# Performance work log

Hardware: AMD Instinct MI355X
Metric: run time of the kernel (lower is better)

Reference implementation:

```python
import jax, jax.numpy as jnp
import numpy as np

B, CIN, OUT = 16, 64, 64
CH = CIN // 2          # depthwise group count (32)
H, W = 256, 256        # mas resolution; cen is at (H//2, W//2)

# The 8 fixed 3x3 dilation-3 kernels are center-minus-shifted-neighbor ops.
# Cross-correlation offsets (dy, dx) of the -1 tap, dilation 3:
OFFSETS = [(-3, -3), (-3, 0), (-3, 3), (0, 3), (3, 3), (3, 0), (3, -3), (0, -3)]


def setup_inputs() -> dict:
    key = jax.random.key(0)
    ks = jax.random.split(key, 9)
    cen = jax.random.normal(ks[0], (B, CIN, H // 2, W // 2), jnp.float32)
    mas = jax.random.normal(ks[1], (B, CH, H, W), jnp.float32)
    # inp_layer: Conv2d(CH, CH, k=3, s=2, p=1) + SiLU
    w_inp = jax.random.normal(ks[2], (CH, CH, 3, 3), jnp.float32) * 0.05
    b_inp = jax.random.normal(ks[3], (CH,), jnp.float32) * 0.05
    # layer1/2/3: grouped 1x1, groups=CH, per-group 8 in -> 2 out; store as [CH, 2, 8]
    w1 = jax.random.normal(ks[4], (CH, 2, 8), jnp.float32) * 0.1
    w2 = jax.random.normal(ks[5], (CH, 2, 8), jnp.float32) * 0.1
    w3 = jax.random.normal(ks[6], (CH, 2, 8), jnp.float32) * 0.1
    # out_conv: 1x1 conv, 3*CIN -> OUT, with bias
    w_out = jax.random.normal(ks[7], (OUT, 3 * CIN), jnp.float32) * 0.05
    b_out = jax.random.normal(ks[8], (OUT,), jnp.float32) * 0.05
    return {"cen": cen, "mas": mas, "w_inp": w_inp, "b_inp": b_inp,
            "w1": w1, "w2": w2, "w3": w3, "w_out": w_out, "b_out": b_out}


def _forward(cen, mas, w_inp, b_inp, w1, w2, w3, w_out, b_out):
    # stem: 3x3 stride-2 conv + SiLU  -> [B, CH, H//2, W//2]
    x = jax.lax.conv_general_dilated(
        mas, w_inp, window_strides=(2, 2), padding=((1, 1), (1, 1)),
        dimension_numbers=("NCHW", "OIHW", "NCHW"))
    x = jax.nn.silu(x + b_inp[None, :, None, None])
    b, c, h, w = x.shape
    # 8 dilated depthwise diff-convs == center minus zero-padded shifted copy
    xp = jnp.pad(x, ((0, 0), (0, 0), (3, 3), (3, 3)))
    deltas = jnp.stack(
        [x - jax.lax.dynamic_slice(xp, (0, 0, 3 + dy, 3 + dx), (b, c, h, w))
         for dy, dx in OFFSETS], axis=2)                     # [B, CH, 8, h, w]
    # grouped 1x1 gating convs (groups=CH): per-group [2,8] matmul
    g1 = jnp.einsum("bcdhw,cod->bcohw", deltas, w1)
    g2 = jnp.einsum("bcdhw,cod->bcohw", deltas, w2)
    square = (g1 * g2).reshape(b, 2 * c, h, w)               # layer1 * layer2
    dout = jnp.einsum("bcdhw,cod->bcohw", deltas, w3).reshape(b, 2 * c, h, w)
    # concat [square, dout, cen] along channels -> 1x1 out_conv
    outs = jnp.concatenate([square, dout, cen], axis=1)      # [B, 3*CIN, h, w]
    return jnp.einsum("bchw,oc->bohw", outs, w_out) + b_out[None, :, None, None]


def reference(cen, mas, w_inp, b_inp, w1, w2, w3, w_out, b_out):
    return _forward(cen, mas, w_inp, b_inp, w1, w2, w3, w_out, b_out)
```

## Files before the change

kernel.cpp:

```cpp
#include <hip/hip_runtime.h>
#include <hip/hip_bf16.h>

#define BATCH 16
#define CH    32
#define CIN   64
#define OUTC  64
#define HH    128
#define WW    128
#define HW    (HH * WW)
#define MHW   65536

typedef __attribute__((ext_vector_type(8))) short bf16x8;
typedef __attribute__((ext_vector_type(4))) float f32x4;

__device__ inline unsigned short bf16u(float x) {
  union { __hip_bfloat16 h; unsigned short s; } u;
  u.h = __float2bfloat16(x);
  return u.s;
}
__device__ inline unsigned int pack2(float lo, float hi) {
  return (unsigned int)bf16u(lo) | ((unsigned int)bf16u(hi) << 16);
}
__device__ inline float losf(unsigned u) { return __uint_as_float(u << 16); }
__device__ inline float hisf(unsigned u) { return __uint_as_float(u & 0xffff0000u); }

__global__ __launch_bounds__(256) void k_prep_weights(
    const float* __restrict__ w_out, const float* __restrict__ w_inp,
    const float* __restrict__ w3,
    unsigned short* __restrict__ wfrag, unsigned short* __restrict__ wfrag2,
    unsigned short* __restrict__ wfrag3) {
  int t = blockIdx.x * 256 + threadIdx.x;
  if (t < 9 * 2 * 64 * 8) {
    int e    = t & 7;
    int lane = (t >> 3) & 63;
    int ct   = (t >> 9) & 1;
    int tap  = t >> 10;
    int co = ct * 16 + (lane & 15);
    int ci = (lane >> 4) * 8 + e;
    wfrag[t] = bf16u(w_inp[(co * CH + ci) * 9 + tap]);
  }
  int t2 = t - 9216;
  if (t2 >= 0 && t2 < 8192) {
    int e    = t2 & 7;
    int lane = (t2 >> 3) & 63;
    int ot   = (t2 >> 9) & 3;
    int kt   = t2 >> 11;
    int o = ot * 16 + (lane & 15);
    int k = kt * 32 + (lane >> 4) * 8 + e;
    int col = (k < 64) ? k : 64 + k;
    wfrag2[t2] = bf16u(w_out[o * 192 + col]);
  }
  int t3 = t - 17408;
  if (t3 >= 0 && t3 < 18432) {
    int e    = t3 & 7;
    int lane = (t3 >> 3) & 63;
    int ot   = (t3 >> 9) & 3;
    int tap  = t3 >> 11;
    int o = ot * 16 + (lane & 15);
    int C = (lane >> 4) * 8 + e;
    const int kmap[9] = {0, 1, 2, 7, -1, 3, 6, 5, 4};
    float v = 0.f;
    if (tap == 4) {
      for (int k = 0; k < 8; ++k)
        for (int op = 0; op < 2; ++op)
          v += w_out[o * 192 + 64 + 2 * C + op] * w3[C * 16 + op * 8 + k];
    } else {
      int k = kmap[tap];
      for (int op = 0; op < 2; ++op)
        v -= w_out[o * 192 + 64 + 2 * C + op] * w3[C * 16 + op * 8 + k];
    }
    wfrag3[t3] = bf16u(v);
  }
}

__global__ __launch_bounds__(256) void k_prep_mas(
    const float* __restrict__ mas, unsigned short* __restrict__ masb) {
  __shared__ alignas(16) unsigned short tile[256 * 36];

  const int W = blockIdx.x + 256 * blockIdx.y;
  const int F = (W & 7) * 512 + (W >> 3);
  const int r = F & 255;
  const int b = F >> 8;
  const int t = threadIdx.x;

  const float* gp = mas + (size_t)b * CH * MHW + (size_t)r * 256 + t;
#pragma unroll 8
  for (int q = 0; q < 16; ++q) {
    float v0 = gp[(size_t)(2 * q) * MHW];
    float v1 = gp[(size_t)(2 * q + 1) * MHW];
    *(unsigned*)&tile[t * 36 + 2 * q] = pack2(v0, v1);
  }
  __syncthreads();

  unsigned short* op = masb + (((size_t)b * 256 + r) * 256) * 32;
#pragma unroll
  for (int it = 0; it < 4; ++it) {
    int idx = it * 256 + t;
    int px = idx >> 2, seg = idx & 3;
    uint2 a  = *(const uint2*)&tile[px * 36 + seg * 8];
    uint2 bq = *(const uint2*)&tile[px * 36 + seg * 8 + 4];
    *(uint4*)(op + (size_t)px * 32 + seg * 8) = make_uint4(a.x, a.y, bq.x, bq.y);
  }
}

#define SPITCH 36

__global__ __launch_bounds__(256, 3) void k_stem(
    const unsigned short* __restrict__ masb,
    const unsigned short* __restrict__ wfrag,
    const float* __restrict__ b_inp, unsigned short* __restrict__ xbuf) {
  __shared__ alignas(16) unsigned short xs[585 * SPITCH];

  const int W = blockIdx.x + 4 * blockIdx.y + 128 * blockIdx.z;
  const int F = (W & 7) * 256 + (W >> 3);
  const int bx = F & 3;
  const int by = (F >> 2) & 31;
  const int b  = F >> 7;

  const int t  = threadIdx.x;
  const int lane = t & 63;
  const int w = t >> 6;
  const int ct = w >> 1, chh = w & 1;

  const int I0 = by * 4, J0 = bx * 32;
  const int R0 = 2 * I0 - 1, C0 = 2 * J0 - 1;

  bf16x8 af[9];
#pragma unroll
  for (int tap = 0; tap < 9; ++tap)
    af[tap] = ((const bf16x8*)wfrag)[(tap * 2 + ct) * 64 + lane];

  const unsigned short* mb = masb + (size_t)b * 256 * 256 * 32;
  for (int idx = t; idx < 585 * 4; idx += 256) {
    int px = idx >> 2, seg = idx & 3;
    int rr = px / 65, cc = px - rr * 65;
    int gr = R0 + rr, gc = C0 + cc;
    uint4 v = make_uint4(0u, 0u, 0u, 0u);
    if (gr >= 0 && gc >= 0)
      v = *(const uint4*)(mb + ((size_t)gr * 256 + gc) * 32 + seg * 8);
    unsigned short* sp = xs + px * SPITCH + seg * 8;
    *(uint2*)(sp)     = make_uint2(v.x, v.y);
    *(uint2*)(sp + 4) = make_uint2(v.z, v.w);
  }
  __syncthreads();

  f32x4 acc[4];
#pragma unroll
  for (int il = 0; il < 4; ++il) acc[il] = 0.f;

  const int jt = chh * 16 + (lane & 15);
  const int gsh = (lane >> 4) * 8;

#pragma unroll
  for (int ky = 0; ky < 3; ++ky) {
#pragma unroll
    for (int kx = 0; kx < 3; ++kx) {
      const int tap = ky * 3 + kx;
#pragma unroll
      for (int il = 0; il < 4; ++il) {
        int pix = (2 * il + ky) * 65 + 2 * jt + kx;
        bf16x8 bfr = *(const bf16x8*)(xs + pix * SPITCH + gsh);
        acc[il] = __builtin_amdgcn_mfma_f32_16x16x32_bf16(
            af[tap], bfr, acc[il], 0, 0, 0);
      }
    }
  }

  float4 bia = *(const float4*)(b_inp + ct * 16 + (lane >> 4) * 4);
  const int co0 = ct * 16 + (lane >> 4) * 4;
  const int colg = J0 + jt;
#pragma unroll
  for (int il = 0; il < 4; ++il) {
    int i = I0 + il;
    float y0 = acc[il][0] + bia.x;
    float y1 = acc[il][1] + bia.y;
    float y2 = acc[il][2] + bia.z;
    float y3 = acc[il][3] + bia.w;
    float s0 = y0 / (1.f + __expf(-y0));
    float s1 = y1 / (1.f + __expf(-y1));
    float s2 = y2 / (1.f + __expf(-y2));
    float s3 = y3 / (1.f + __expf(-y3));
    uint2 uv;
    uv.x = pack2(s0, s1);
    uv.y = pack2(s2, s3);
    *(uint2*)(xbuf + ((size_t)(b * HH + i) * WW + colg) * 32 + co0) = uv;
  }
}

#define PPITCH 132

__global__ __launch_bounds__(256, 4) void k_fused(
    const unsigned short* __restrict__ xbuf, const float* __restrict__ cen,
    const float* __restrict__ w1, const float* __restrict__ w2,
    const unsigned short* __restrict__ wfrag2,
    const unsigned short* __restrict__ wfrag3,
    const float* __restrict__ b_out, float* __restrict__ out) {
  __shared__ alignas(16) unsigned short xs[196 * 36];
  __shared__ alignas(16) unsigned short panel[64][PPITCH];

  const int W = blockIdx.x + 16 * blockIdx.y + 256 * blockIdx.z;
  const int F = (W & 7) * 512 + (W >> 3);
  const int bx = F & 15;
  const int by = (F >> 4) & 15;
  const int b  = F >> 8;

  const int t  = threadIdx.x;
  const int lane = t & 63;
  const int w = t >> 6;
  const int I0 = by * 8, J0 = bx * 8;

  bf16x8 af3[9], af2[4];
#pragma unroll
  for (int tap = 0; tap < 9; ++tap)
    af3[tap] = ((const bf16x8*)wfrag3)[(tap * 4 + w) * 64 + lane];
#pragma unroll
  for (int kt = 0; kt < 4; ++kt)
    af2[kt] = ((const bf16x8*)wfrag2)[(kt * 4 + w) * 64 + lane];

#pragma unroll
  for (int j = 0; j < 8; ++j) {
    int idx = j * 256 + t;
    int cc = idx >> 6, p = idx & 63;
    int py = p >> 3, px = p & 7;
    const float* cp = cen + ((size_t)(b * CIN + 2 * cc) * HH + I0 + py) * WW
                      + J0 + px;
    *(unsigned int*)&panel[p][64 + 2 * cc] = pack2(cp[0], cp[HW]);
  }

  {
    int row = t >> 4, col = t & 15;
    if (row < 14 && col < 14) {
      int gi = I0 - 3 + row, gj = J0 - 3 + col;
      bool ok = (gi >= 0 && gi < HH && gj >= 0 && gj < WW);
      const unsigned short* gp = xbuf +
          ((size_t)((size_t)b * HH + (ok ? gi : 0)) * WW + (ok ? gj : 0)) * 32;
      unsigned short* sp = xs + (row * 14 + col) * 36;
#pragma unroll
      for (int s = 0; s < 4; ++s) {
        uint4 v = make_uint4(0u, 0u, 0u, 0u);
        if (ok) v = *(const uint4*)(gp + 8 * s);
        *(uint2*)(sp + 8 * s)     = make_uint2(v.x, v.y);
        *(uint2*)(sp + 8 * s + 4) = make_uint2(v.z, v.w);
      }
    }
  }
  __syncthreads();

  f32x4 acc[4];
#pragma unroll
  for (int pt = 0; pt < 4; ++pt) acc[pt] = 0.f;

  const int prow = lane & 15;
  const int gsh = (lane >> 4) * 8;
#pragma unroll
  for (int pt = 0; pt < 4; ++pt) {
    int p = pt * 16 + prow;
    int ppy = p >> 3, ppx = p & 7;
#pragma unroll
    for (int ty = 0; ty < 3; ++ty)
#pragma unroll
      for (int tx = 0; tx < 3; ++tx) {
        int pos = (ppy + 3 * ty) * 14 + ppx + 3 * tx;
        bf16x8 bfr = *(const bf16x8*)(xs + pos * 36 + gsh);
        acc[pt] = __builtin_amdgcn_mfma_f32_16x16x32_bf16(
            af3[ty * 3 + tx], bfr, acc[pt], 0, 0, 0);
      }
  }

  {
    const int py = lane >> 3, px = lane & 7;
    const int posc = (py + 3) * 14 + (px + 3);
    int pos8[8];
    pos8[0] = (py + 0) * 14 + px + 0;
    pos8[1] = (py + 0) * 14 + px + 3;
    pos8[2] = (py + 0) * 14 + px + 6;
    pos8[3] = (py + 3) * 14 + px + 6;
    pos8[4] = (py + 6) * 14 + px + 6;
    pos8[5] = (py + 6) * 14 + px + 3;
    pos8[6] = (py + 6) * 14 + px + 0;
    pos8[7] = (py + 3) * 14 + px + 0;

#pragma unroll
    for (int j = 0; j < 4; ++j) {
      int c2 = __builtin_amdgcn_readfirstlane(j * 4 + w);
      const float* w1lo = w1 + (2 * c2) * 16;
      const float* w1hi = w1 + (2 * c2 + 1) * 16;
      const float* w2lo = w2 + (2 * c2) * 16;
      const float* w2hi = w2 + (2 * c2 + 1) * 16;
      unsigned uc = *(const unsigned*)(xs + posc * 36 + 2 * c2);
      float clo = losf(uc), chi = hisf(uc);
      float g1l0 = 0, g1l1 = 0, g2l0 = 0, g2l1 = 0;
      float g1h0 = 0, g1h1 = 0, g2h0 = 0, g2h1 = 0;
#pragma unroll
      for (int k = 0; k < 8; ++k) {
        unsigned us = *(const unsigned*)(xs + pos8[k] * 36 + 2 * c2);
        float dlo = clo - losf(us);
        float dhi = chi - hisf(us);
        g1l0 += dlo * w1lo[k];  g1l1 += dlo * w1lo[8 + k];
        g2l0 += dlo * w2lo[k];  g2l1 += dlo * w2lo[8 + k];
        g1h0 += dhi * w1hi[k];  g1h1 += dhi * w1hi[8 + k];
        g2h0 += dhi * w2hi[k];  g2h1 += dhi * w2hi[8 + k];
      }
      uint2 wv;
      wv.x = pack2(g1l0 * g2l0, g1l1 * g2l1);
      wv.y = pack2(g1h0 * g2h0, g1h1 * g2h1);
      *(uint2*)&panel[lane][4 * c2] = wv;
    }
  }
  __syncthreads();

#pragma unroll
  for (int pt = 0; pt < 4; ++pt) {
#pragma unroll
    for (int kt = 0; kt < 4; ++kt) {
      bf16x8 bfr = *(const bf16x8*)(&panel[pt * 16 + prow][kt * 32 + gsh]);
      acc[pt] = __builtin_amdgcn_mfma_f32_16x16x32_bf16(
          af2[kt], bfr, acc[pt], 0, 0, 0);
    }
  }

  float4 bo = *(const float4*)(b_out + w * 16 + (lane >> 4) * 4);
#pragma unroll
  for (int pt = 0; pt < 4; ++pt) {
    int p = pt * 16 + prow;
    int ppy = p >> 3, ppx = p & 7;
#pragma unroll
    for (int r = 0; r < 4; ++r) {
      int o = w * 16 + (lane >> 4) * 4 + r;
      out[((b * OUTC + o) * HH + I0 + ppy) * WW + J0 + ppx] =
          acc[pt][r] + ((const float*)&bo)[r];
    }
  }
}

extern "C" void kernel_launch(void* const* d_in, const int* in_sizes, int n_in,
                              void* d_out, int out_size, void* d_ws, size_t ws_size,
                              hipStream_t stream) {
  const float* cen   = (const float*)d_in[0];
  const float* mas   = (const float*)d_in[1];
  const float* w_inp = (const float*)d_in[2];
  const float* b_inp = (const float*)d_in[3];
  const float* w1    = (const float*)d_in[4];
  const float* w2    = (const float*)d_in[5];
  const float* w3    = (const float*)d_in[6];
  const float* w_out = (const float*)d_in[7];
  const float* b_out = (const float*)d_in[8];
  float* out = (float*)d_out;

  unsigned short* masb   = (unsigned short*)d_ws;
  unsigned short* xbuf   = masb + (size_t)BATCH * 256 * 256 * 32;
  unsigned short* wfrag  = xbuf + (size_t)BATCH * HW * 32;
  unsigned short* wfrag2 = wfrag + 9216;
  unsigned short* wfrag3 = wfrag2 + 8192;

  hipLaunchKernelGGL(k_prep_mas, dim3(256, 16), dim3(256), 0, stream,
                     mas, masb);
  hipLaunchKernelGGL(k_prep_weights, dim3(140), dim3(256), 0, stream,
                     w_out, w_inp, w3, wfrag, wfrag2, wfrag3);
  hipLaunchKernelGGL(k_stem, dim3(4, 32, 16), dim3(256), 0, stream,
                     masb, wfrag, b_inp, xbuf);
  hipLaunchKernelGGL(k_fused, dim3(16, 16, 16), dim3(256), 0, stream,
                     xbuf, cen, w1, w2, wfrag2, wfrag3, b_out, out);
}
```

Before: 117.0 us.

## Fuse mas NCHW-to-bf16 transpose into stem conv and retile stem blocks

```diff
diff --git a/kernel.cpp b/kernel.cpp
--- a/kernel.cpp
+++ b/kernel.cpp
@@ -73,83 +73,55 @@
   }
 }
 
-__global__ __launch_bounds__(256) void k_prep_mas(
-    const float* __restrict__ mas, unsigned short* __restrict__ masb) {
-  __shared__ alignas(16) unsigned short tile[256 * 36];
-
-  const int W = blockIdx.x + 256 * blockIdx.y;
-  const int F = (W & 7) * 512 + (W >> 3);
-  const int r = F & 255;
-  const int b = F >> 8;
-  const int t = threadIdx.x;
-
-  const float* gp = mas + (size_t)b * CH * MHW + (size_t)r * 256 + t;
-#pragma unroll 8
-  for (int q = 0; q < 16; ++q) {
-    float v0 = gp[(size_t)(2 * q) * MHW];
-    float v1 = gp[(size_t)(2 * q + 1) * MHW];
-    *(unsigned*)&tile[t * 36 + 2 * q] = pack2(v0, v1);
-  }
-  __syncthreads();
-
-  unsigned short* op = masb + (((size_t)b * 256 + r) * 256) * 32;
-#pragma unroll
-  for (int it = 0; it < 4; ++it) {
-    int idx = it * 256 + t;
-    int px = idx >> 2, seg = idx & 3;
-    uint2 a  = *(const uint2*)&tile[px * 36 + seg * 8];
-    uint2 bq = *(const uint2*)&tile[px * 36 + seg * 8 + 4];
-    *(uint4*)(op + (size_t)px * 32 + seg * 8) = make_uint4(a.x, a.y, bq.x, bq.y);
-  }
-}
-
-#define SPITCH 36
-
 __global__ __launch_bounds__(256, 3) void k_stem(
-    const unsigned short* __restrict__ masb,
-    const unsigned short* __restrict__ wfrag,
+    const float* __restrict__ mas, const unsigned short* __restrict__ wfrag,
     const float* __restrict__ b_inp, unsigned short* __restrict__ xbuf) {
-  __shared__ alignas(16) unsigned short xs[585 * SPITCH];
-
-  const int W = blockIdx.x + 4 * blockIdx.y + 128 * blockIdx.z;
+  __shared__ alignas(16) unsigned int xs32[645 * 18];
+
+  const int W = blockIdx.x + 2 * blockIdx.y + 128 * blockIdx.z;
   const int F = (W & 7) * 256 + (W >> 3);
-  const int bx = F & 3;
-  const int by = (F >> 2) & 31;
+  const int bx = F & 1;
+  const int by = (F >> 1) & 63;
   const int b  = F >> 7;
 
   const int t  = threadIdx.x;
   const int lane = t & 63;
   const int w = t >> 6;
-  const int ct = w >> 1, chh = w & 1;
-
-  const int I0 = by * 4, J0 = bx * 32;
+
+  const int I0 = by * 2, J0 = bx * 64;
   const int R0 = 2 * I0 - 1, C0 = 2 * J0 - 1;
 
-  bf16x8 af[9];
+  bf16x8 af[9][2];
 #pragma unroll
   for (int tap = 0; tap < 9; ++tap)
-    af[tap] = ((const bf16x8*)wfrag)[(tap * 2 + ct) * 64 + lane];
-
-  const unsigned short* mb = masb + (size_t)b * 256 * 256 * 32;
-  for (int idx = t; idx < 585 * 4; idx += 256) {
-    int px = idx >> 2, seg = idx & 3;
-    int rr = px / 65, cc = px - rr * 65;
-    int gr = R0 + rr, gc = C0 + cc;
-    uint4 v = make_uint4(0u, 0u, 0u, 0u);
-    if (gr >= 0 && gc >= 0)
-      v = *(const uint4*)(mb + ((size_t)gr * 256 + gc) * 32 + seg * 8);
-    unsigned short* sp = xs + px * SPITCH + seg * 8;
-    *(uint2*)(sp)     = make_uint2(v.x, v.y);
-    *(uint2*)(sp + 4) = make_uint2(v.z, v.w);
+#pragma unroll
+    for (int ct = 0; ct < 2; ++ct)
+      af[tap][ct] = ((const bf16x8*)wfrag)[(tap * 2 + ct) * 64 + lane];
+
+  const float* mb = mas + (size_t)b * CH * MHW;
+  for (int idx = t; idx < 80 * 129; idx += 256) {
+    int cell = idx / 129;
+    int col  = idx - cell * 129;
+    int r  = cell >> 4;
+    int cp = cell & 15;
+    int gr = R0 + r, gc = C0 + col;
+    unsigned v = 0u;
+    if (gr >= 0 && gc >= 0) {
+      const float* p = mb + (size_t)(2 * cp) * MHW + (size_t)gr * 256 + gc;
+      v = pack2(p[0], p[MHW]);
+    }
+    xs32[(r * 129 + col) * 18 + cp] = v;
   }
   __syncthreads();
 
-  f32x4 acc[4];
-#pragma unroll
-  for (int il = 0; il < 4; ++il) acc[il] = 0.f;
-
-  const int jt = chh * 16 + (lane & 15);
-  const int gsh = (lane >> 4) * 8;
+  f32x4 acc[2][2];
+#pragma unroll
+  for (int il = 0; il < 2; ++il)
+#pragma unroll
+    for (int ct = 0; ct < 2; ++ct) acc[il][ct] = 0.f;
+
+  const int jt = w * 16 + (lane & 15);
+  const int g4 = (lane >> 4) * 4;
 
 #pragma unroll
   for (int ky = 0; ky < 3; ++ky) {
@@ -157,33 +129,40 @@
     for (int kx = 0; kx < 3; ++kx) {
       const int tap = ky * 3 + kx;
 #pragma unroll
-      for (int il = 0; il < 4; ++il) {
-        int pix = (2 * il + ky) * 65 + 2 * jt + kx;
-        bf16x8 bfr = *(const bf16x8*)(xs + pix * SPITCH + gsh);
-        acc[il] = __builtin_amdgcn_mfma_f32_16x16x32_bf16(
-            af[tap], bfr, acc[il], 0, 0, 0);
+      for (int il = 0; il < 2; ++il) {
+        int pix = (2 * il + ky) * 129 + 2 * jt + kx;
+        bf16x8 bfr = *(const bf16x8*)(xs32 + pix * 18 + g4);
+        acc[il][0] = __builtin_amdgcn_mfma_f32_16x16x32_bf16(
+            af[tap][0], bfr, acc[il][0], 0, 0, 0);
+        acc[il][1] = __builtin_amdgcn_mfma_f32_16x16x32_bf16(
+            af[tap][1], bfr, acc[il][1], 0, 0, 0);
       }
     }
   }
 
-  float4 bia = *(const float4*)(b_inp + ct * 16 + (lane >> 4) * 4);
-  const int co0 = ct * 16 + (lane >> 4) * 4;
+  float4 bia[2];
+  bia[0] = *(const float4*)(b_inp + (lane >> 4) * 4);
+  bia[1] = *(const float4*)(b_inp + 16 + (lane >> 4) * 4);
   const int colg = J0 + jt;
 #pragma unroll
-  for (int il = 0; il < 4; ++il) {
+  for (int il = 0; il < 2; ++il) {
     int i = I0 + il;
-    float y0 = acc[il][0] + bia.x;
-    float y1 = acc[il][1] + bia.y;
-    float y2 = acc[il][2] + bia.z;
-    float y3 = acc[il][3] + bia.w;
-    float s0 = y0 / (1.f + __expf(-y0));
-    float s1 = y1 / (1.f + __expf(-y1));
-    float s2 = y2 / (1.f + __expf(-y2));
-    float s3 = y3 / (1.f + __expf(-y3));
-    uint2 uv;
-    uv.x = pack2(s0, s1);
-    uv.y = pack2(s2, s3);
-    *(uint2*)(xbuf + ((size_t)(b * HH + i) * WW + colg) * 32 + co0) = uv;
+#pragma unroll
+    for (int ct = 0; ct < 2; ++ct) {
+      int co0 = ct * 16 + (lane >> 4) * 4;
+      float y0 = acc[il][ct][0] + ((const float*)&bia[ct])[0];
+      float y1 = acc[il][ct][1] + ((const float*)&bia[ct])[1];
+      float y2 = acc[il][ct][2] + ((const float*)&bia[ct])[2];
+      float y3 = acc[il][ct][3] + ((const float*)&bia[ct])[3];
+      float s0 = y0 / (1.f + __expf(-y0));
+      float s1 = y1 / (1.f + __expf(-y1));
+      float s2 = y2 / (1.f + __expf(-y2));
+      float s3 = y3 / (1.f + __expf(-y3));
+      uint2 uv;
+      uv.x = pack2(s0, s1);
+      uv.y = pack2(s2, s3);
+      *(uint2*)(xbuf + ((size_t)(b * HH + i) * WW + colg) * 32 + co0) = uv;
+    }
   }
 }
 
@@ -347,18 +326,15 @@
   const float* b_out = (const float*)d_in[8];
   float* out = (float*)d_out;
 
-  unsigned short* masb   = (unsigned short*)d_ws;
-  unsigned short* xbuf   = masb + (size_t)BATCH * 256 * 256 * 32;
+  unsigned short* xbuf   = (unsigned short*)d_ws;
   unsigned short* wfrag  = xbuf + (size_t)BATCH * HW * 32;
   unsigned short* wfrag2 = wfrag + 9216;
   unsigned short* wfrag3 = wfrag2 + 8192;
 
-  hipLaunchKernelGGL(k_prep_mas, dim3(256, 16), dim3(256), 0, stream,
-                     mas, masb);
   hipLaunchKernelGGL(k_prep_weights, dim3(140), dim3(256), 0, stream,
                      w_out, w_inp, w3, wfrag, wfrag2, wfrag3);
-  hipLaunchKernelGGL(k_stem, dim3(4, 32, 16), dim3(256), 0, stream,
-                     masb, wfrag, b_inp, xbuf);
+  hipLaunchKernelGGL(k_stem, dim3(2, 64, 16), dim3(256), 0, stream,
+                     mas, wfrag, b_inp, xbuf);
   hipLaunchKernelGGL(k_fused, dim3(16, 16, 16), dim3(256), 0, stream,
                      xbuf, cen, w1, w2, wfrag2, wfrag3, b_out, out);
 }
```

Result: slower. 140.8 us (+20.3%).
